# Optimization experiments

Measured on AMD Instinct MI355X. Metric: run time of the kernel, lower is better.

Reference implementation:

```python
import jax, jax.numpy as jnp
import numpy as np

D_MODEL = 1024
N_HEADS = 16
HEAD_DIM = D_MODEL // N_HEADS
SCALE = HEAD_DIM ** -0.5
NEG = -9e15


def setup_inputs() -> dict:
    key = jax.random.key(0)
    k1, k2, k3 = jax.random.split(key, 3)
    B, S = 4, 2048
    x = jax.random.normal(k1, (B, S, D_MODEL), dtype=jnp.float32)
    W_qkv = jax.random.normal(k2, (D_MODEL, 3 * D_MODEL), dtype=jnp.float32) * (D_MODEL ** -0.5)
    b_qkv = jnp.zeros((3 * D_MODEL,), dtype=jnp.float32)
    W_out = jax.random.normal(k3, (D_MODEL, D_MODEL), dtype=jnp.float32) * (D_MODEL ** -0.5)
    b_out = jnp.zeros((D_MODEL,), dtype=jnp.float32)
    return {"x": x, "W_qkv": W_qkv, "b_qkv": b_qkv, "W_out": W_out, "b_out": b_out}


def reference(x, W_qkv, b_qkv, W_out, b_out):
    B, S, _ = x.shape
    qkv = x @ W_qkv + b_qkv                      # [B,S,3D]
    q, k, v = jnp.split(qkv, 3, axis=-1)
    def heads(t):
        return t.reshape(B, S, N_HEADS, HEAD_DIM).transpose(0, 2, 1, 3)  # [B,H,S,d]
    q, k, v = heads(q), heads(k), heads(v)
    logits = jnp.einsum('bhqd,bhkd->bhqk', q, k) * SCALE
    causal = jnp.tril(jnp.ones((S, S), dtype=bool))
    logits = jnp.where(causal[None, None], logits, jnp.float32(NEG))
    attn = jax.nn.softmax(logits, axis=-1)       # dropout p=0 -> identity
    vals = jnp.einsum('bhqk,bhkd->bhqd', attn, v)
    vals = vals.transpose(0, 2, 1, 3).reshape(B, S, D_MODEL)
    return vals @ W_out + b_out
```

## Files before the change

kernel.cpp:

```cpp
#include <hip/hip_runtime.h>

typedef unsigned short u16;
typedef unsigned int u32;
typedef __attribute__((ext_vector_type(8))) short bf16x8;
typedef __attribute__((ext_vector_type(4))) float f32x4;

#define MFMA16(a, b, c) __builtin_amdgcn_mfma_f32_16x16x32_bf16((a), (b), (c), 0, 0, 0)

constexpr int D = 1024;
constexpr int NH = 16;
constexpr int HD = 64;
constexpr int BB = 4;
constexpr int SS = 2048;
constexpr int BH = BB * NH;
constexpr int MTOK = BB * SS;
constexpr float SCALE_LOG2E = 0.125f * 1.44269504088896340736f;

__device__ __forceinline__ u16 f32_bf16(float f) {
  union { float f; u32 u; } v; v.f = f;
  u32 u = v.u;
  u += 0x7FFFu + ((u >> 16) & 1u);
  return (u16)(u >> 16);
}

__device__ __forceinline__ float exp2_fast(float x) {
  float r; asm("v_exp_f32 %0, %1" : "=v"(r) : "v"(x)); return r;
}
__device__ __forceinline__ u16 cvt_bf16_1(float f) {
  u32 r; asm("v_cvt_pk_bf16_f32 %0, %1, %1" : "=v"(r) : "v"(f)); return (u16)r;
}
__device__ __forceinline__ u32 cvt_pk2(float lo, float hi) {
  u32 r; asm("v_cvt_pk_bf16_f32 %0, %1, %2" : "=v"(r) : "v"(lo), "v"(hi)); return r;
}

__device__ __forceinline__ void gload_lds16(const void* g, u16* l) {
  __builtin_amdgcn_global_load_lds(
      (const __attribute__((address_space(1))) u32*)g,
      (__attribute__((address_space(3))) u32*)l, 16, 0, 0);
}

__global__ __launch_bounds__(256)
void cvt_bf16(const float* __restrict__ in, u16* __restrict__ out, int n4) {
  int i = blockIdx.x * 256 + threadIdx.x;
  const int stride = gridDim.x * 256;
  for (; i < n4; i += stride) {
    float4 v = reinterpret_cast<const float4*>(in)[i];
    u32 lo = (u32)f32_bf16(v.x) | ((u32)f32_bf16(v.y) << 16);
    u32 hi = (u32)f32_bf16(v.z) | ((u32)f32_bf16(v.w) << 16);
    reinterpret_cast<uint2*>(out)[i] = make_uint2(lo, hi);
  }
}

__global__ __launch_bounds__(256)
void transpose_bf16(const float* __restrict__ in, u16* __restrict__ out, int R, int C) {
  __shared__ float tile[32][33];
  const int c0 = blockIdx.x * 32, r0 = blockIdx.y * 32;
  const int tx = threadIdx.x, ty = threadIdx.y;
#pragma unroll
  for (int i = 0; i < 4; i++)
    tile[ty + 8 * i][tx] = in[(size_t)(r0 + ty + 8 * i) * C + c0 + tx];
  __syncthreads();
#pragma unroll
  for (int i = 0; i < 4; i++)
    out[(size_t)(c0 + ty + 8 * i) * R + r0 + tx] = f32_bf16(tile[tx][ty + 8 * i]);
}

template <int MODE>
__global__ __launch_bounds__(512)
void gemm_bf16(const u16* __restrict__ A, const u16* __restrict__ Bt,
               const float* __restrict__ bias,
               u16* __restrict__ q_out, u16* __restrict__ k_out,
               u16* __restrict__ vt_out, float* __restrict__ f_out,
               int M, int N, int K) {
  constexpr int BK = 64;
  __shared__ u16 lds_a[2][16384];
  __shared__ u16 lds_b[2][8192];
  const int m0 = blockIdx.x * 256;
  const int n0 = blockIdx.y * 128;
  const int t = threadIdx.x;
  const int lane = t & 63;
  const int w = t >> 6;
  const int wr = w >> 1, wc = w & 1;
  const int fr = lane & 15, fq = lane >> 4;

  const int srow = t >> 2;
  const int schunk = (t & 3) ^ ((t >> 3) & 3);
  const u16* ga0 = A + (size_t)(m0 + srow) * K + schunk * 8;
  const u16* ga1 = A + (size_t)(m0 + 128 + srow) * K + schunk * 8;
  const u16* ga2 = ga0 + 32;
  const u16* ga3 = ga1 + 32;
  const u16* gb0 = Bt + (size_t)(n0 + srow) * K + schunk * 8;
  const u16* gb1 = gb0 + 32;
  const int t8 = t * 8;

  const int rswz = ((fr >> 1) & 3) << 4;

#define GSTAGE(bufi, kt)                                                      \
  {                                                                           \
    const int ko = (kt)*BK;                                                   \
    gload_lds16(ga0 + ko, lds_a[bufi] + t8);                                  \
    gload_lds16(ga1 + ko, lds_a[bufi] + 4096 + t8);                           \
    gload_lds16(ga2 + ko, lds_a[bufi] + 8192 + t8);                           \
    gload_lds16(ga3 + ko, lds_a[bufi] + 12288 + t8);                          \
    gload_lds16(gb0 + ko, lds_b[bufi] + t8);                                  \
    gload_lds16(gb1 + ko, lds_b[bufi] + 4096 + t8);                           \
  }

  f32x4 acc[4][4] = {};
  const int nt = K / BK;

  GSTAGE(0, 0);
  int cur = 0;
  for (int kt = 0; kt < nt; ++kt) {
    if (kt) {
      __builtin_amdgcn_s_barrier();
      __builtin_amdgcn_sched_barrier(0);
    }
    if (kt + 1 < nt) GSTAGE(cur ^ 1, kt + 1);
    if (kt + 1 < nt)
      asm volatile("s_waitcnt vmcnt(6)" ::: "memory");
    else
      asm volatile("s_waitcnt vmcnt(0)" ::: "memory");
    __builtin_amdgcn_s_barrier();
    __builtin_amdgcn_sched_barrier(0);

    const char* ca = (const char*)lds_a[cur];
    const char* cb = (const char*)lds_b[cur];
#pragma unroll
    for (int ks = 0; ks < 2; ks++) {
      bf16x8 af[4], bf[4];
#pragma unroll
      for (int i = 0; i < 4; i++)
        af[i] = *reinterpret_cast<const bf16x8*>(
            ca + ks * 16384 + (wr * 64 + i * 16 + fr) * 64 + ((fq * 16) ^ rswz));
#pragma unroll
      for (int j = 0; j < 4; j++)
        bf[j] = *reinterpret_cast<const bf16x8*>(
            cb + ks * 8192 + (wc * 64 + j * 16 + fr) * 64 + ((fq * 16) ^ rswz));
      __builtin_amdgcn_s_setprio(1);
#pragma unroll
      for (int i = 0; i < 4; i++)
#pragma unroll
        for (int j = 0; j < 4; j++)
          acc[i][j] = MFMA16(af[i], bf[j], acc[i][j]);
      __builtin_amdgcn_s_setprio(0);
    }
    cur ^= 1;
  }
#undef GSTAGE

  if (MODE == 0) {
    const int swhich = n0 >> 10;
#pragma unroll
    for (int i = 0; i < 4; i++) {
#pragma unroll
      for (int j = 0; j < 4; j++) {
        const int ncol = n0 + wc * 64 + j * 16 + fr;
        const float bs = bias[ncol];
        const int rem = ncol & 1023;
        const int hh = rem >> 6, dd = rem & 63;
        const int mbase = m0 + wr * 64 + i * 16 + fq * 4;
        const int bb = mbase >> 11, ss = mbase & 2047;
        const int bh = bb * 16 + hh;
        if (swhich == 0) {
#pragma unroll
          for (int r = 0; r < 4; r++)
            q_out[((size_t)bh * SS + ss + r) * HD + dd] =
                f32_bf16((acc[i][j][r] + bs) * SCALE_LOG2E);
        } else if (swhich == 1) {
#pragma unroll
          for (int r = 0; r < 4; r++)
            k_out[((size_t)bh * SS + ss + r) * HD + dd] = f32_bf16(acc[i][j][r] + bs);
        } else {
          const u32 p01 = cvt_pk2(acc[i][j][0] + bs, acc[i][j][1] + bs);
          const u32 p23 = cvt_pk2(acc[i][j][2] + bs, acc[i][j][3] + bs);
          *reinterpret_cast<uint2*>(&vt_out[((size_t)bh * HD + dd) * SS + ss]) =
              make_uint2(p01, p23);
        }
      }
    }
  } else {
#pragma unroll
    for (int i = 0; i < 4; i++) {
#pragma unroll
      for (int j = 0; j < 4; j++) {
        const int ncol = n0 + wc * 64 + j * 16 + fr;
        const float bs = bias[ncol];
#pragma unroll
        for (int r = 0; r < 4; r++) {
          const int mrow = m0 + wr * 64 + i * 16 + fq * 4 + r;
          f_out[(size_t)mrow * N + ncol] = acc[i][j][r] + bs;
        }
      }
    }
  }
}

__global__ __launch_bounds__(512)
void attn_fwd(const u16* __restrict__ Qb, const u16* __restrict__ Kb,
              const u16* __restrict__ Vt, u16* __restrict__ vals) {
  const int bid = blockIdx.x;
  const int wk = (bid & 7) * 64 + (bid >> 3);
  const int bh = wk >> 3;
  const int pA = wk & 7;
  const int qtA = pA, qtB = 15 - pA;
  const int nA = 2 * qtA + 2;
  const int nTot = 34;
  const u16* Qp = Qb + (size_t)bh * SS * HD;
  const char* Kp = (const char*)(Kb + (size_t)bh * SS * HD);
  const char* Vp = (const char*)(Vt + (size_t)bh * HD * SS);
  const int t = threadIdx.x, lane = t & 63, w = t >> 6;
  const int fr = lane & 15, fq = lane >> 4;
  const int swz = (fr & 7) << 4;

  __shared__ u16 kbuf[3][4096];
  __shared__ u16 vbuf[3][4096];
  __shared__ u16 plds[8][16][72];
  u16* myp = &plds[w][0][0];

  const int lin = t * 16;

  int offKV[8];
#pragma unroll
  for (int kf = 0; kf < 4; kf++)
#pragma unroll
    for (int kk = 0; kk < 2; kk++)
      offKV[kf * 2 + kk] = (kf * 16 + fr) * 128 + ((kk * 64 + fq * 16) ^ swz);

  bf16x8 aq[2];
  {
    const int qbase = qtA * 128 + w * 16;
#pragma unroll
    for (int kk = 0; kk < 2; kk++)
      aq[kk] = *reinterpret_cast<const bf16x8*>(Qp + (size_t)(qbase + fr) * HD + kk * 32 + fq * 8);
  }

  f32x4 o[4] = {};
  float mrun = -3e38f, lpart = 0.f;

#define STAGE(bufi, kvt_)                                                     \
  {                                                                           \
    const int row = lin >> 7, colb = lin & 127;                               \
    const int scol = colb ^ ((row & 7) << 4);                                 \
    gload_lds16(Kp + (size_t)((kvt_) * 64 + row) * 128 + scol,                \
                &kbuf[bufi][lin >> 1]);                                       \
    gload_lds16(Vp + (size_t)row * 4096 + (kvt_) * 128 + scol,                \
                &vbuf[bufi][lin >> 1]);                                       \
  }
#define KVIDX(ti_) ((ti_) >= nA ? (ti_) - nA : (ti_))

  auto write_out = [&](int qt) {
    const int b_ = bh >> 4, h_ = bh & 15;
    const int qb = qt * 128 + w * 16;
    float rs = lpart;
    rs += __shfl_xor(rs, 16, 64);
    rs += __shfl_xor(rs, 32, 64);
    const float linv = 1.f / rs;
    float lj[4];
#pragma unroll
    for (int j = 0; j < 4; j++)
      lj[j] = __shfl(linv, (lane & 48) + fq * 4 + j, 64);
#pragma unroll
    for (int df = 0; df < 4; df++)
#pragma unroll
      for (int j = 0; j < 4; j++) {
        const float vv = o[df][j] * lj[j];
        const int qg = qb + fq * 4 + j;
        vals[((size_t)(b_ * SS + qg)) * D + h_ * HD + df * 16 + fr] = cvt_bf16_1(vv);
      }
  };

  int cur = 0;
  STAGE(0, 0);
  STAGE(1, 1);

  for (int ti = 0; ti < nTot; ++ti) {
    const bool segB = ti >= nA;
    const int kvt = segB ? ti - nA : ti;
    const int qt = segB ? qtB : qtA;

    if (ti + 1 < nTot)
      asm volatile("s_waitcnt vmcnt(2)" ::: "memory");
    else
      asm volatile("s_waitcnt vmcnt(0)" ::: "memory");
    __builtin_amdgcn_s_barrier();
    __builtin_amdgcn_sched_barrier(0);

    if (ti == nA) {
      write_out(qtA);
      const int qbase = qtB * 128 + w * 16;
#pragma unroll
      for (int kk = 0; kk < 2; kk++)
        aq[kk] = *reinterpret_cast<const bf16x8*>(Qp + (size_t)(qbase + fr) * HD + kk * 32 + fq * 8);
      mrun = -3e38f; lpart = 0.f;
#pragma unroll
      for (int df = 0; df < 4; df++) o[df] = f32x4{0.f, 0.f, 0.f, 0.f};
    }

    const char* kb = (const char*)kbuf[cur];
    const char* vb = (const char*)vbuf[cur];

    f32x4 sc[4] = {};
    __builtin_amdgcn_s_setprio(1);
#pragma unroll
    for (int kf = 0; kf < 4; kf++) {
#pragma unroll
      for (int kk = 0; kk < 2; kk++) {
        bf16x8 bk = *reinterpret_cast<const bf16x8*>(kb + offKV[kf * 2 + kk]);
        sc[kf] = MFMA16(bk, aq[kk], sc[kf]);
      }
    }
    __builtin_amdgcn_s_setprio(0);
    if ((kvt >> 1) == qt) {
      const int qg = qt * 128 + w * 16 + fr;
      const int kg0 = kvt * 64 + fq * 4;
#pragma unroll
      for (int kf = 0; kf < 4; kf++)
#pragma unroll
        for (int j = 0; j < 4; j++)
          if (kg0 + kf * 16 + j > qg) sc[kf][j] = -3e38f;
    }
    float m = fmaxf(fmaxf(sc[0][0], sc[0][1]), fmaxf(sc[0][2], sc[0][3]));
#pragma unroll
    for (int kf = 1; kf < 4; kf++)
      m = fmaxf(m, fmaxf(fmaxf(sc[kf][0], sc[kf][1]), fmaxf(sc[kf][2], sc[kf][3])));
    m = fmaxf(m, __shfl_xor(m, 16, 64));
    m = fmaxf(m, __shfl_xor(m, 32, 64));
    if (__any((int)(m > mrun + 8.f))) {
      const float mnew = fmaxf(mrun, m);
      const float alpha = exp2_fast(mrun - mnew);
      mrun = mnew;
      lpart *= alpha;
      float aj[4];
#pragma unroll
      for (int j = 0; j < 4; j++)
        aj[j] = __shfl(alpha, (lane & 48) + fq * 4 + j, 64);
#pragma unroll
      for (int df = 0; df < 4; df++)
#pragma unroll
        for (int j = 0; j < 4; j++) o[df][j] *= aj[j];
    }
#pragma unroll
    for (int kf = 0; kf < 4; kf++)
#pragma unroll
      for (int j = 0; j < 4; j++) {
        const float p = exp2_fast(sc[kf][j] - mrun);
        sc[kf][j] = p;
        lpart += p;
      }
    {
      u16* mypr = myp + fr * 72;
#pragma unroll
      for (int kf = 0; kf < 4; kf++) {
        const u32 p01 = cvt_pk2(sc[kf][0], sc[kf][1]);
        const u32 p23 = cvt_pk2(sc[kf][2], sc[kf][3]);
        *reinterpret_cast<u32*>(mypr + kf * 16 + fq * 4) = p01;
        *reinterpret_cast<u32*>(mypr + kf * 16 + fq * 4 + 2) = p23;
      }
    }
    bf16x8 pa[2];
#pragma unroll
    for (int kk = 0; kk < 2; kk++)
      pa[kk] = *reinterpret_cast<const bf16x8*>(myp + fr * 72 + kk * 32 + fq * 8);
    __builtin_amdgcn_s_setprio(1);
#pragma unroll
    for (int df = 0; df < 4; df++) {
#pragma unroll
      for (int kk = 0; kk < 2; kk++) {
        bf16x8 bv = *reinterpret_cast<const bf16x8*>(vb + offKV[df * 2 + kk]);
        o[df] = MFMA16(pa[kk], bv, o[df]);
      }
    }
    __builtin_amdgcn_s_setprio(0);

    const int nxt = ti + 2;
    if (nxt < nTot) {
      const int bufn = cur >= 1 ? cur - 1 : 2;
      STAGE(bufn, KVIDX(nxt));
    }
    cur = cur == 2 ? 0 : cur + 1;
  }
  write_out(qtB);
#undef STAGE
#undef KVIDX
}

extern "C" void kernel_launch(void* const* d_in, const int* in_sizes, int n_in,
                              void* d_out, int out_size, void* d_ws, size_t ws_size,
                              hipStream_t stream) {
  const float* x = (const float*)d_in[0];
  const float* Wqkv = (const float*)d_in[1];
  const float* bqkv = (const float*)d_in[2];
  const float* Wout = (const float*)d_in[3];
  const float* bout = (const float*)d_in[4];
  float* out = (float*)d_out;

  char* p = (char*)d_ws;
  u16* xb = (u16*)p;    p += (size_t)MTOK * D * 2;
  u16* wqkvT = (u16*)p; p += (size_t)3 * D * D * 2;
  u16* woutT = (u16*)p; p += (size_t)D * D * 2;
  u16* Qb = (u16*)p;    p += (size_t)BH * SS * HD * 2;
  u16* Kb = (u16*)p;    p += (size_t)BH * SS * HD * 2;
  u16* Vt = (u16*)p;    p += (size_t)BH * SS * HD * 2;
  u16* vals = (u16*)p;  p += (size_t)MTOK * D * 2;

  cvt_bf16<<<2048, 256, 0, stream>>>(x, xb, MTOK * D / 4);
  transpose_bf16<<<dim3(3 * D / 32, D / 32), dim3(32, 8), 0, stream>>>(Wqkv, wqkvT, D, 3 * D);
  transpose_bf16<<<dim3(D / 32, D / 32), dim3(32, 8), 0, stream>>>(Wout, woutT, D, D);
  gemm_bf16<0><<<dim3(MTOK / 256, 3 * D / 128), 512, 0, stream>>>(
      xb, wqkvT, bqkv, Qb, Kb, Vt, nullptr, MTOK, 3 * D, D);
  attn_fwd<<<dim3(512), 512, 0, stream>>>(Qb, Kb, Vt, vals);
  gemm_bf16<1><<<dim3(MTOK / 256, D / 128), 512, 0, stream>>>(
      vals, woutT, bout, nullptr, nullptr, nullptr, out, MTOK, D, D);
}
```

Measured before the change: 179.0 us.

## Add dedicated 128x128 triple-buffered kernel for the output projection GEMM

```diff
diff --git a/kernel.cpp b/kernel.cpp
--- a/kernel.cpp
+++ b/kernel.cpp
@@ -65,13 +65,11 @@
     out[(size_t)(c0 + ty + 8 * i) * R + r0 + tx] = f32_bf16(tile[tx][ty + 8 * i]);
 }
 
-template <int MODE>
 __global__ __launch_bounds__(512)
-void gemm_bf16(const u16* __restrict__ A, const u16* __restrict__ Bt,
-               const float* __restrict__ bias,
-               u16* __restrict__ q_out, u16* __restrict__ k_out,
-               u16* __restrict__ vt_out, float* __restrict__ f_out,
-               int M, int N, int K) {
+void gemm_qkv(const u16* __restrict__ A, const u16* __restrict__ Bt,
+              const float* __restrict__ bias,
+              u16* __restrict__ q_out, u16* __restrict__ k_out,
+              u16* __restrict__ vt_out, int M, int N, int K) {
   constexpr int BK = 64;
   __shared__ u16 lds_a[2][16384];
   __shared__ u16 lds_b[2][8192];
@@ -149,48 +147,121 @@
   }
 #undef GSTAGE
 
-  if (MODE == 0) {
-    const int swhich = n0 >> 10;
-#pragma unroll
-    for (int i = 0; i < 4; i++) {
-#pragma unroll
-      for (int j = 0; j < 4; j++) {
-        const int ncol = n0 + wc * 64 + j * 16 + fr;
-        const float bs = bias[ncol];
-        const int rem = ncol & 1023;
-        const int hh = rem >> 6, dd = rem & 63;
-        const int mbase = m0 + wr * 64 + i * 16 + fq * 4;
-        const int bb = mbase >> 11, ss = mbase & 2047;
-        const int bh = bb * 16 + hh;
-        if (swhich == 0) {
-#pragma unroll
-          for (int r = 0; r < 4; r++)
-            q_out[((size_t)bh * SS + ss + r) * HD + dd] =
-                f32_bf16((acc[i][j][r] + bs) * SCALE_LOG2E);
-        } else if (swhich == 1) {
-#pragma unroll
-          for (int r = 0; r < 4; r++)
-            k_out[((size_t)bh * SS + ss + r) * HD + dd] = f32_bf16(acc[i][j][r] + bs);
-        } else {
-          const u32 p01 = cvt_pk2(acc[i][j][0] + bs, acc[i][j][1] + bs);
-          const u32 p23 = cvt_pk2(acc[i][j][2] + bs, acc[i][j][3] + bs);
-          *reinterpret_cast<uint2*>(&vt_out[((size_t)bh * HD + dd) * SS + ss]) =
-              make_uint2(p01, p23);
-        }
-      }
-    }
-  } else {
-#pragma unroll
-    for (int i = 0; i < 4; i++) {
-#pragma unroll
-      for (int j = 0; j < 4; j++) {
-        const int ncol = n0 + wc * 64 + j * 16 + fr;
-        const float bs = bias[ncol];
-#pragma unroll
-        for (int r = 0; r < 4; r++) {
-          const int mrow = m0 + wr * 64 + i * 16 + fq * 4 + r;
-          f_out[(size_t)mrow * N + ncol] = acc[i][j][r] + bs;
-        }
+  const int swhich = n0 >> 10;
+#pragma unroll
+  for (int i = 0; i < 4; i++) {
+#pragma unroll
+    for (int j = 0; j < 4; j++) {
+      const int ncol = n0 + wc * 64 + j * 16 + fr;
+      const float bs = bias[ncol];
+      const int rem = ncol & 1023;
+      const int hh = rem >> 6, dd = rem & 63;
+      const int mbase = m0 + wr * 64 + i * 16 + fq * 4;
+      const int bb = mbase >> 11, ss = mbase & 2047;
+      const int bh = bb * 16 + hh;
+      if (swhich == 0) {
+#pragma unroll
+        for (int r = 0; r < 4; r++)
+          q_out[((size_t)bh * SS + ss + r) * HD + dd] =
+              f32_bf16((acc[i][j][r] + bs) * SCALE_LOG2E);
+      } else if (swhich == 1) {
+#pragma unroll
+        for (int r = 0; r < 4; r++)
+          k_out[((size_t)bh * SS + ss + r) * HD + dd] = f32_bf16(acc[i][j][r] + bs);
+      } else {
+        const u32 p01 = cvt_pk2(acc[i][j][0] + bs, acc[i][j][1] + bs);
+        const u32 p23 = cvt_pk2(acc[i][j][2] + bs, acc[i][j][3] + bs);
+        *reinterpret_cast<uint2*>(&vt_out[((size_t)bh * HD + dd) * SS + ss]) =
+            make_uint2(p01, p23);
+      }
+    }
+  }
+}
+
+__global__ __launch_bounds__(256)
+void gemm_proj(const u16* __restrict__ A, const u16* __restrict__ Bt,
+               const float* __restrict__ bias, float* __restrict__ f_out,
+               int M, int N, int K) {
+  constexpr int BK = 32;
+  __shared__ u16 lds_a[3][128 * BK];
+  __shared__ u16 lds_b[3][128 * BK];
+  const int m0 = blockIdx.x * 128;
+  const int n0 = blockIdx.y * 128;
+  const int t = threadIdx.x;
+  const int lane = t & 63;
+  const int w = t >> 6;
+  const int wr = w >> 1, wc = w & 1;
+  const int fr = lane & 15, fq = lane >> 4;
+
+  const int srow = t >> 2;
+  const int schunk = (t & 3) ^ ((srow >> 1) & 3);
+  const u16* ga0 = A + (size_t)(m0 + srow) * K + schunk * 8;
+  const u16* ga1 = ga0 + (size_t)64 * K;
+  const u16* gb0 = Bt + (size_t)(n0 + srow) * K + schunk * 8;
+  const u16* gb1 = gb0 + (size_t)64 * K;
+
+  const int swz = ((fr >> 1) & 3) << 4;
+
+#define GSTAGE(bufi, koff)                                                    \
+  {                                                                           \
+    gload_lds16(ga0 + (koff), lds_a[bufi] + t * 8);                           \
+    gload_lds16(ga1 + (koff), lds_a[bufi] + (t + 256) * 8);                   \
+    gload_lds16(gb0 + (koff), lds_b[bufi] + t * 8);                           \
+    gload_lds16(gb1 + (koff), lds_b[bufi] + (t + 256) * 8);                   \
+  }
+
+  f32x4 acc[4][4] = {};
+  const int nt = K / BK;
+
+  GSTAGE(0, 0);
+  GSTAGE(1, BK);
+
+  int cur = 0;
+  for (int kt = 0; kt < nt; ++kt) {
+    if (kt + 1 < nt)
+      asm volatile("s_waitcnt vmcnt(4)" ::: "memory");
+    else
+      asm volatile("s_waitcnt vmcnt(0)" ::: "memory");
+    __builtin_amdgcn_s_barrier();
+    __builtin_amdgcn_sched_barrier(0);
+
+    const char* ca = (const char*)lds_a[cur];
+    const char* cb = (const char*)lds_b[cur];
+    bf16x8 af[4], bfr[4];
+#pragma unroll
+    for (int i = 0; i < 4; i++)
+      af[i] = *reinterpret_cast<const bf16x8*>(
+          ca + (wr * 64 + i * 16 + fr) * 64 + ((fq * 16) ^ swz));
+#pragma unroll
+    for (int i = 0; i < 4; i++)
+      bfr[i] = *reinterpret_cast<const bf16x8*>(
+          cb + (wc * 64 + i * 16 + fr) * 64 + ((fq * 16) ^ swz));
+    __builtin_amdgcn_s_setprio(1);
+#pragma unroll
+    for (int i = 0; i < 4; i++)
+#pragma unroll
+      for (int j = 0; j < 4; j++)
+        acc[i][j] = MFMA16(af[i], bfr[j], acc[i][j]);
+    __builtin_amdgcn_s_setprio(0);
+
+    if (kt + 2 < nt) {
+      const int bufn = cur >= 1 ? cur - 1 : 2;
+      GSTAGE(bufn, (kt + 2) * BK);
+    }
+    cur = cur == 2 ? 0 : cur + 1;
+  }
+#undef GSTAGE
+
+#pragma unroll
+  for (int i = 0; i < 4; i++) {
+#pragma unroll
+    for (int j = 0; j < 4; j++) {
+      const int ncol = n0 + wc * 64 + j * 16 + fr;
+      const float bs = bias[ncol];
+#pragma unroll
+      for (int r = 0; r < 4; r++) {
+        const int mrow = m0 + wr * 64 + i * 16 + fq * 4 + r;
+        f_out[(size_t)mrow * N + ncol] = acc[i][j][r] + bs;
       }
     }
   }
@@ -407,9 +478,9 @@
   cvt_bf16<<<2048, 256, 0, stream>>>(x, xb, MTOK * D / 4);
   transpose_bf16<<<dim3(3 * D / 32, D / 32), dim3(32, 8), 0, stream>>>(Wqkv, wqkvT, D, 3 * D);
   transpose_bf16<<<dim3(D / 32, D / 32), dim3(32, 8), 0, stream>>>(Wout, woutT, D, D);
-  gemm_bf16<0><<<dim3(MTOK / 256, 3 * D / 128), 512, 0, stream>>>(
-      xb, wqkvT, bqkv, Qb, Kb, Vt, nullptr, MTOK, 3 * D, D);
+  gemm_qkv<<<dim3(MTOK / 256, 3 * D / 128), 512, 0, stream>>>(
+      xb, wqkvT, bqkv, Qb, Kb, Vt, MTOK, 3 * D, D);
   attn_fwd<<<dim3(512), 512, 0, stream>>>(Qb, Kb, Vt, vals);
-  gemm_bf16<1><<<dim3(MTOK / 256, D / 128), 512, 0, stream>>>(
-      vals, woutT, bout, nullptr, nullptr, nullptr, out, MTOK, D, D);
-}
+  gemm_proj<<<dim3(MTOK / 128, D / 128), 256, 0, stream>>>(
+      vals, woutT, bout, out, MTOK, D, D);
+}
```

New measurement: 175.6 us. About the same (-1.9%).
